# Optimization experiments

Measured on AMD Instinct MI355X. Metric: run time of the kernel, lower is better.

Reference implementation:

```python
import jax, jax.numpy as jnp
import numpy as np

T, B, N, F = 128, 8, 32, 128
H = 256  # hidden channels
DEG = 8


def setup_inputs() -> dict:
    key = jax.random.key(0)
    ks = jax.random.split(key, 8)
    data = jax.random.normal(ks[0], (T, B, N, F), jnp.float32)
    all_ohs = jax.random.normal(ks[1], (T, B, N, 8), jnp.float32)
    n0 = B * N * T
    n1 = B * N * (T // 2)
    edge_index0 = jax.random.randint(ks[2], (2, n0 * DEG), 0, n0)
    edge_index1 = jax.random.randint(ks[3], (2, n1 * DEG), 0, n1)
    def init(k, shape, fan):
        return jax.random.normal(k, shape, jnp.float32) / np.float32(np.sqrt(fan))
    W0 = init(ks[4], (2 * F, H), 2 * F); b0 = jnp.zeros((H,), jnp.float32)
    Wc0 = init(ks[5], (H, H, 5), H * 5); bc0 = jnp.zeros((H,), jnp.float32)
    W1 = init(ks[6], (2 * H, H), 2 * H); b1 = jnp.zeros((H,), jnp.float32)
    Wc1 = init(ks[7], (H, H, 5), H * 5); bc1 = jnp.zeros((H,), jnp.float32)
    return dict(data=data, all_ohs=all_ohs,
                edge_index0=edge_index0, edge_index1=edge_index1,
                W0=W0, b0=b0, Wc0=Wc0, bc0=bc0,
                W1=W1, b1=b1, Wc1=Wc1, bc1=bc1)


def edge_conv(x, edge_index, W, b):
    # PyG EdgeConv: out_i = max_{(j->i)} relu(Linear(cat[x_i, x_j - x_i]))
    src, dst = edge_index[0], edge_index[1]
    x_i = x[dst]           # [E, C] target features
    x_j = x[src]           # [E, C] source features
    msg = jax.nn.relu(jnp.concatenate([x_i, x_j - x_i], axis=-1) @ W + b)
    out = jax.ops.segment_max(msg, dst, num_segments=x.shape[0])
    return jnp.where(jnp.isneginf(out), 0.0, out)  # empty segments -> 0 (PyG fill)


def temp_conv(x, Wc, bc):
    # x: [BN, C, L]; Conv1d(k=5, pad=2) + relu + MaxPool1d(2)
    y = jax.lax.conv_general_dilated(x, Wc, (1,), [(2, 2)],
                                     dimension_numbers=('NCH', 'OIH', 'NCH'))
    y = jax.nn.relu(y + bc[None, :, None])
    L2 = y.shape[-1] // 2
    y = y[..., : L2 * 2].reshape(y.shape[0], y.shape[1], L2, 2)
    return jnp.max(y, axis=-1)


def reference(data, all_ohs, edge_index0, edge_index1,
              W0, b0, Wc0, bc0, W1, b1, Wc1, bc1):
    # 'fast' path, context=False: all_ohs unused beyond reshape
    length = data.shape[0]
    x = data.reshape(T, B * N, F).transpose(1, 0, 2).reshape(-1, F)  # [BN*T, F]
    layers = ((edge_index0, W0, b0, Wc0, bc0),
              (edge_index1, W1, b1, Wc1, bc1))
    for ei, W, b, Wc, bc in layers:
        x = edge_conv(x, ei, W, b)                       # [BN*length, C]
        x = x.reshape(-1, length, x.shape[-1])           # [BN, length, C]
        x = x.transpose(0, 2, 1)                         # [BN, C, length]
        x = temp_conv(x, Wc, bc)                         # [BN, C, length//2]
        length = x.shape[2]
        C = x.shape[1]
        x = x.transpose(0, 2, 1).reshape(-1, C)          # [BN*length, C]
    return x
```

## Files before the change

kernel.cpp:

```cpp
#include <hip/hip_runtime.h>
#include <hip/hip_bf16.h>
#include <math.h>

#define T0 128
#define BN 256
#define Ff 128
#define Hh 256
#define NODE0 32768
#define E0 262144
#define T1 64
#define NODE1 16384
#define E1 131072
#define CAP 48

typedef __attribute__((ext_vector_type(8))) short bhalf8;
typedef __attribute__((ext_vector_type(4))) float floatx4;
typedef __attribute__((ext_vector_type(16))) float floatx16;

__device__ __forceinline__ unsigned short f2bf(float x) {
  union { float f; unsigned u; } v; v.f = x;
  unsigned r = v.u + 0x7fff + ((v.u >> 16) & 1);
  return (unsigned short)(r >> 16);
}
__device__ __forceinline__ float bf2f(unsigned short b) {
  union { unsigned u; float f; } v; v.u = ((unsigned)b) << 16;
  return v.f;
}

__global__ void k_prepfill(const float* __restrict__ data, unsigned short* __restrict__ X0b,
                           const float* __restrict__ W0, unsigned short* __restrict__ Wbot0,
                           unsigned short* __restrict__ Wd0,
                           const float* __restrict__ W1, unsigned short* __restrict__ Wbot1,
                           unsigned short* __restrict__ Wd1,
                           const float* __restrict__ Wc0, unsigned short* __restrict__ Wtb0,
                           const float* __restrict__ Wc1, unsigned short* __restrict__ Wtb1,
                           const int* __restrict__ ei0, const int* __restrict__ ei1,
                           int* __restrict__ cnt0, int* __restrict__ cnt1,
                           int* __restrict__ slot0, int* __restrict__ slot1) {
  int b = blockIdx.x;
  int tid = threadIdx.x;
  if (b < 2048) {
    int idx = b * 256 + tid;
    int c8 = idx & 15;
    int r  = idx >> 4;
    int t  = r & (T0 - 1);
    int bn = r >> 7;
    const float* s = data + ((size_t)t * BN + bn) * Ff + c8 * 8;
    float4 a = *(const float4*)s;
    float4 bb = *(const float4*)(s + 4);
    unsigned short o[8];
    o[0] = f2bf(a.x); o[1] = f2bf(a.y); o[2] = f2bf(a.z); o[3] = f2bf(a.w);
    o[4] = f2bf(bb.x); o[5] = f2bf(bb.y); o[6] = f2bf(bb.z); o[7] = f2bf(bb.w);
    *(int4*)(X0b + ((size_t)(bn * T0 + t) * Ff + c8 * 8)) = *(int4*)o;
  } else if (b < 2176) {
    int idx = (b - 2048) * 256 + tid;
    int n = idx >> 7, k = idx & 127;
    float top = W0[(size_t)k * 256 + n];
    float bot = W0[(size_t)(128 + k) * 256 + n];
    Wbot0[idx] = f2bf(bot);
    Wd0[idx]   = f2bf(top - bot);
  } else if (b < 2432) {
    int idx = (b - 2176) * 256 + tid;
    int n = idx >> 8, k = idx & 255;
    float top = W1[(size_t)k * 256 + n];
    float bot = W1[(size_t)(256 + k) * 256 + n];
    Wbot1[idx] = f2bf(bot);
    Wd1[idx]   = f2bf(top - bot);
  } else if (b < 3712) {
    int idx = (b - 2432) * 256 + tid;
    int tap = idx >> 16, o = (idx >> 8) & 255, i = idx & 255;
    Wtb0[idx] = f2bf(Wc0[((size_t)o * 256 + i) * 5 + tap]);
  } else if (b < 4992) {
    int idx = (b - 3712) * 256 + tid;
    int tap = idx >> 16, o = (idx >> 8) & 255, i = idx & 255;
    Wtb1[idx] = f2bf(Wc1[((size_t)o * 256 + i) * 5 + tap]);
  } else {
    int e = (b - 4992) * 256 + tid;
    if (e < E0) {
      int d = ei0[E0 + e];
      int p = atomicAdd(&cnt0[d], 1);
      if (p < CAP) slot0[(size_t)d * CAP + p] = ei0[e];
    } else {
      int e2 = e - E0;
      int d = ei1[E1 + e2];
      int p = atomicAdd(&cnt1[d], 1);
      if (p < CAP) slot1[(size_t)d * CAP + p] = ei1[e2];
    }
  }
}

__global__ __launch_bounds__(256) void k_gemm2(const unsigned short* __restrict__ A,
                                               const unsigned short* __restrict__ Wbot,
                                               const unsigned short* __restrict__ Wd,
                                               unsigned short* __restrict__ Bm,
                                               unsigned short* __restrict__ P, int K,
                                               const float* __restrict__ bias) {
  __shared__ __align__(16) short A_lds[128 * 72];
  __shared__ __align__(16) short B0_lds[128 * 72];
  __shared__ __align__(16) short B1_lds[128 * 72];
  int tid = threadIdx.x;
  int row0 = blockIdx.x * 128;
  int col0 = blockIdx.y * 128;
  int lane = tid & 63, wv = tid >> 6;
  int m16 = lane & 15, quad = lane >> 4;
  int sr = tid >> 3, sseg = tid & 7;

  floatx4 accB[2][8], accP[2][8];
#pragma unroll
  for (int rt = 0; rt < 2; ++rt)
#pragma unroll
    for (int nt = 0; nt < 8; ++nt) {
      accB[rt][nt] = (floatx4){0.f, 0.f, 0.f, 0.f};
      accP[rt][nt] = (floatx4){0.f, 0.f, 0.f, 0.f};
    }

  for (int kb = 0; kb < K; kb += 64) {
    __syncthreads();
#pragma unroll
    for (int i = 0; i < 4; ++i) {
      int r = sr + i * 32;
      *(int4*)&A_lds[r * 72 + sseg * 8] =
          *(const int4*)(A + (size_t)(row0 + r) * K + kb + sseg * 8);
      *(int4*)&B0_lds[r * 72 + sseg * 8] =
          *(const int4*)(Wbot + (size_t)(col0 + r) * K + kb + sseg * 8);
      *(int4*)&B1_lds[r * 72 + sseg * 8] =
          *(const int4*)(Wd + (size_t)(col0 + r) * K + kb + sseg * 8);
    }
    __syncthreads();
#pragma unroll
    for (int ks = 0; ks < 2; ++ks) {
      bhalf8 a0 = *(const bhalf8*)&A_lds[(wv * 32 + m16) * 72 + ks * 32 + quad * 8];
      bhalf8 a1 = *(const bhalf8*)&A_lds[(wv * 32 + 16 + m16) * 72 + ks * 32 + quad * 8];
#pragma unroll
      for (int nt = 0; nt < 8; ++nt) {
        bhalf8 b0 = *(const bhalf8*)&B0_lds[(nt * 16 + m16) * 72 + ks * 32 + quad * 8];
        accB[0][nt] = __builtin_amdgcn_mfma_f32_16x16x32_bf16(a0, b0, accB[0][nt], 0, 0, 0);
        accB[1][nt] = __builtin_amdgcn_mfma_f32_16x16x32_bf16(a1, b0, accB[1][nt], 0, 0, 0);
        bhalf8 b1 = *(const bhalf8*)&B1_lds[(nt * 16 + m16) * 72 + ks * 32 + quad * 8];
        accP[0][nt] = __builtin_amdgcn_mfma_f32_16x16x32_bf16(a0, b1, accP[0][nt], 0, 0, 0);
        accP[1][nt] = __builtin_amdgcn_mfma_f32_16x16x32_bf16(a1, b1, accP[1][nt], 0, 0, 0);
      }
    }
  }

#pragma unroll
  for (int rt = 0; rt < 2; ++rt) {
    int g0 = row0 + wv * 32 + rt * 16 + quad * 4;
#pragma unroll
    for (int nt = 0; nt < 8; ++nt) {
      int c = col0 + nt * 16 + m16;
      float bv = bias[c];
#pragma unroll
      for (int r = 0; r < 4; ++r) {
        Bm[(size_t)(g0 + r) * 256 + c] = f2bf(accB[rt][nt][r]);
        P[(size_t)(g0 + r) * 256 + c]  = f2bf(accP[rt][nt][r] + bv);
      }
    }
  }
}

__global__ __launch_bounds__(256) void k_maxg2(const unsigned short* __restrict__ Bm,
                                               const int* __restrict__ cnt,
                                               const int* __restrict__ slot,
                                               const unsigned short* __restrict__ P,
                                               unsigned short* __restrict__ X1) {
  int node = blockIdx.x * 4 + (threadIdx.x >> 6);
  int lane = threadIdx.x & 63;
  int n = cnt[node];
  if (n > CAP) n = CAP;
  const int* sl = slot + (size_t)node * CAP;
  float4 m = make_float4(-INFINITY, -INFINITY, -INFINITY, -INFINITY);
  for (int i = 0; i < n; i += 8) {
    int s[8];
#pragma unroll
    for (int j = 0; j < 8; ++j) {
      int idx = i + j;
      s[j] = sl[(idx < n) ? idx : (n - 1)];
    }
    ushort4 v[8];
#pragma unroll
    for (int j = 0; j < 8; ++j)
      v[j] = *(const ushort4*)(Bm + (size_t)s[j] * 256 + lane * 4);
#pragma unroll
    for (int j = 0; j < 8; ++j) {
      m.x = fmaxf(m.x, bf2f(v[j].x));
      m.y = fmaxf(m.y, bf2f(v[j].y));
      m.z = fmaxf(m.z, bf2f(v[j].z));
      m.w = fmaxf(m.w, bf2f(v[j].w));
    }
  }
  ushort4 p = *(const ushort4*)(P + (size_t)node * 256 + lane * 4);
  ushort4 o;
  o.x = f2bf(fmaxf(bf2f(p.x) + m.x, 0.f));
  o.y = f2bf(fmaxf(bf2f(p.y) + m.y, 0.f));
  o.z = f2bf(fmaxf(bf2f(p.z) + m.z, 0.f));
  o.w = f2bf(fmaxf(bf2f(p.w) + m.w, 0.f));
  *(ushort4*)(X1 + (size_t)node * 256 + lane * 4) = o;
}

template <int TRows, int NT, bool OUT_F32>
__global__ __launch_bounds__(256) void k_conv32(const unsigned short* __restrict__ X,
                                                const unsigned short* __restrict__ Wtb,
                                                const float* __restrict__ bc,
                                                void* __restrict__ Yout) {
  const int CB = NT * 64;
  __shared__ __align__(16) short A_lds[2 * 68 * 40];
  __shared__ __align__(16) short B_lds[5 * CB * 40];
  int tid = threadIdx.x;
  int row0 = blockIdx.x * 128;
  int col0 = blockIdx.y * CB;
  int lane = tid & 63, wv = tid >> 6;
  int l31 = lane & 31, khalf = lane >> 5;
  int h = wv & 1, cpart = wv >> 1;

  floatx16 acc[2][NT];
#pragma unroll
  for (int rt = 0; rt < 2; ++rt)
#pragma unroll
    for (int ct = 0; ct < NT; ++ct)
#pragma unroll
      for (int r = 0; r < 16; ++r) acc[rt][ct][r] = 0.f;

  for (int kb = 0; kb < 256; kb += 32) {
    __syncthreads();
    for (int u = tid; u < 544; u += 256) {
      int s = (u >= 272) ? 1 : 0;
      int v = u - s * 272;
      int rr = v >> 2, seg = v & 3;
      int base = row0 + s * 64;
      int lo = base & ~(TRows - 1);
      int gr = base + rr - 2;
      int4 val = {0, 0, 0, 0};
      if (gr >= lo && gr < lo + TRows)
        val = *(const int4*)(X + (size_t)gr * 256 + kb + seg * 8);
      *(int4*)&A_lds[(s * 68 + rr) * 40 + seg * 8] = val;
    }
#pragma unroll
    for (int i = 0; i < 5 * NT; ++i) {
      int u = tid + i * 256;
      int r = u >> 2, seg = u & 3;
      int tap = r / CB, col = r % CB;
      *(int4*)&B_lds[r * 40 + seg * 8] =
          *(const int4*)(Wtb + (size_t)tap * 65536 + (size_t)(col0 + col) * 256 + kb + seg * 8);
    }
    __syncthreads();
#pragma unroll
    for (int tap = 0; tap < 5; ++tap) {
#pragma unroll
      for (int ks = 0; ks < 2; ++ks) {
        int ko = ks * 16 + khalf * 8;
        bhalf8 a[2];
#pragma unroll
        for (int rt = 0; rt < 2; ++rt)
          a[rt] = *(const bhalf8*)&A_lds[(h * 68 + rt * 32 + l31 + tap) * 40 + ko];
#pragma unroll
        for (int ct = 0; ct < NT; ++ct) {
          bhalf8 b = *(const bhalf8*)&B_lds[(tap * CB + cpart * NT * 32 + ct * 32 + l31) * 40 + ko];
#pragma unroll
          for (int rt = 0; rt < 2; ++rt)
            acc[rt][ct] = __builtin_amdgcn_mfma_f32_32x32x16_bf16(a[rt], b, acc[rt][ct], 0, 0, 0);
        }
      }
    }
  }

#pragma unroll
  for (int rt = 0; rt < 2; ++rt) {
#pragma unroll
    for (int ct = 0; ct < NT; ++ct) {
      int c = col0 + cpart * NT * 32 + ct * 32 + l31;
      float bv = bc[c];
#pragma unroll
      for (int r = 0; r < 16; r += 2) {
        int rowg = row0 + h * 64 + rt * 32 + 4 * khalf + 8 * (r >> 2) + (r & 3);
        float y0 = fmaxf(acc[rt][ct][r] + bv, 0.f);
        float y1 = fmaxf(acc[rt][ct][r + 1] + bv, 0.f);
        float p = fmaxf(y0, y1);
        int o = rowg >> 1;
        if (OUT_F32) ((float*)Yout)[(size_t)o * 256 + c] = p;
        else ((unsigned short*)Yout)[(size_t)o * 256 + c] = f2bf(p);
      }
    }
  }
}

extern "C" void kernel_launch(void* const* d_in, const int* in_sizes, int n_in,
                              void* d_out, int out_size, void* d_ws, size_t ws_size,
                              hipStream_t stream) {
  const float* data = (const float*)d_in[0];
  const int* ei0 = (const int*)d_in[2];
  const int* ei1 = (const int*)d_in[3];
  const float* W0  = (const float*)d_in[4];
  const float* b0  = (const float*)d_in[5];
  const float* Wc0 = (const float*)d_in[6];
  const float* bc0 = (const float*)d_in[7];
  const float* W1  = (const float*)d_in[8];
  const float* b1  = (const float*)d_in[9];
  const float* Wc1 = (const float*)d_in[10];
  const float* bc1 = (const float*)d_in[11];
  float* out = (float*)d_out;

  char* base = (char*)d_ws;
  size_t off = 0;
  auto alloc = [&](size_t bytes) { void* p = base + off; off += (bytes + 255) & ~(size_t)255; return p; };
  unsigned short* X0b   = (unsigned short*)alloc((size_t)NODE0 * Ff * 2);
  unsigned short* Bm    = (unsigned short*)alloc((size_t)NODE0 * Hh * 2);
  unsigned short* P     = (unsigned short*)alloc((size_t)NODE0 * Hh * 2);
  unsigned short* X1b   = (unsigned short*)alloc((size_t)NODE0 * Hh * 2);
  unsigned short* Y0b   = (unsigned short*)alloc((size_t)NODE1 * Hh * 2);
  unsigned short* Wbot0 = (unsigned short*)alloc(256 * 128 * 2);
  unsigned short* Wd0   = (unsigned short*)alloc(256 * 128 * 2);
  unsigned short* Wbot1 = (unsigned short*)alloc(256 * 256 * 2);
  unsigned short* Wd1   = (unsigned short*)alloc(256 * 256 * 2);
  unsigned short* Wtb0  = (unsigned short*)alloc(5 * 65536 * 2);
  unsigned short* Wtb1  = (unsigned short*)alloc(5 * 65536 * 2);
  int* cnt0  = (int*)alloc(NODE0 * 4);
  int* cnt1  = (int*)alloc(NODE1 * 4);
  int* slot0 = (int*)alloc((size_t)NODE0 * CAP * 4);
  int* slot1 = (int*)alloc((size_t)NODE1 * CAP * 4);

  hipMemsetAsync(cnt0, 0, (NODE0 + NODE1) * sizeof(int), stream);

  k_prepfill<<<6528, 256, 0, stream>>>(data, X0b, W0, Wbot0, Wd0, W1, Wbot1, Wd1,
                                       Wc0, Wtb0, Wc1, Wtb1,
                                       ei0, ei1, cnt0, cnt1, slot0, slot1);

  k_gemm2<<<dim3(NODE0 / 128, 2), 256, 0, stream>>>(X0b, Wbot0, Wd0, Bm, P, 128, b0);
  k_maxg2<<<NODE0 / 4, 256, 0, stream>>>(Bm, cnt0, slot0, P, X1b);
  k_conv32<128, 2, false><<<dim3(NODE0 / 128, 2), 256, 0, stream>>>(X1b, Wtb0, bc0, Y0b);

  k_gemm2<<<dim3(NODE1 / 128, 2), 256, 0, stream>>>(Y0b, Wbot1, Wd1, Bm, P, 256, b1);
  k_maxg2<<<NODE1 / 4, 256, 0, stream>>>(Bm, cnt1, slot1, P, X1b);
  k_conv32<64, 2, true><<<dim3(NODE1 / 128, 2), 256, 0, stream>>>(X1b, Wtb1, bc1, out);
}
```

Baseline: 219.7 us.

## Register-prefetch next K tile in GEMM and conv, vectorize gather-max and epilogue

Both the edge GEMM and the temporal-conv kernel now load the next K slice into registers while the current slice is being computed, so global-load latency overlaps the MFMA work. The GEMM swaps MFMA operand order so each lane holds four consecutive columns, which lets the epilogue write ushort4 vectors and read the bias as float4. The gather-max kernel loads 16-byte chunks with two half-waves taking alternating neighbours, then combines them with a cross-lane shuffle. The prefetch buffers raise register pressure, which may reduce occupancy, especially in the conv kernel with 5*NT prefetched int4 values.

```diff
diff --git a/kernel.cpp b/kernel.cpp
--- a/kernel.cpp
+++ b/kernel.cpp
@@ -25,6 +25,13 @@
 __device__ __forceinline__ float bf2f(unsigned short b) {
   union { unsigned u; float f; } v; v.u = ((unsigned)b) << 16;
   return v.f;
+}
+__device__ __forceinline__ void max2(float& mlo, float& mhi, int p) {
+  union { unsigned u; float f; } lo, hi;
+  lo.u = ((unsigned)p) << 16;
+  hi.u = ((unsigned)p) & 0xffff0000u;
+  mlo = fmaxf(mlo, lo.f);
+  mhi = fmaxf(mhi, hi.f);
 }
 
 __global__ void k_prepfill(const float* __restrict__ data, unsigned short* __restrict__ X0b,
@@ -105,6 +112,18 @@
   int m16 = lane & 15, quad = lane >> 4;
   int sr = tid >> 3, sseg = tid & 7;
 
+  const unsigned short* Abase  = A    + (size_t)(row0 + sr) * K + sseg * 8;
+  const unsigned short* B0base = Wbot + (size_t)(col0 + sr) * K + sseg * 8;
+  const unsigned short* B1base = Wd   + (size_t)(col0 + sr) * K + sseg * 8;
+
+  int4 ra[4], rb0[4], rb1[4];
+#pragma unroll
+  for (int i = 0; i < 4; ++i) {
+    ra[i]  = *(const int4*)(Abase  + (size_t)i * 32 * K);
+    rb0[i] = *(const int4*)(B0base + (size_t)i * 32 * K);
+    rb1[i] = *(const int4*)(B1base + (size_t)i * 32 * K);
+  }
+
   floatx4 accB[2][8], accP[2][8];
 #pragma unroll
   for (int rt = 0; rt < 2; ++rt)
@@ -119,12 +138,17 @@
 #pragma unroll
     for (int i = 0; i < 4; ++i) {
       int r = sr + i * 32;
-      *(int4*)&A_lds[r * 72 + sseg * 8] =
-          *(const int4*)(A + (size_t)(row0 + r) * K + kb + sseg * 8);
-      *(int4*)&B0_lds[r * 72 + sseg * 8] =
-          *(const int4*)(Wbot + (size_t)(col0 + r) * K + kb + sseg * 8);
-      *(int4*)&B1_lds[r * 72 + sseg * 8] =
-          *(const int4*)(Wd + (size_t)(col0 + r) * K + kb + sseg * 8);
+      *(int4*)&A_lds[r * 72 + sseg * 8]  = ra[i];
+      *(int4*)&B0_lds[r * 72 + sseg * 8] = rb0[i];
+      *(int4*)&B1_lds[r * 72 + sseg * 8] = rb1[i];
+    }
+    if (kb + 64 < K) {
+#pragma unroll
+      for (int i = 0; i < 4; ++i) {
+        ra[i]  = *(const int4*)(Abase  + (size_t)i * 32 * K + kb + 64);
+        rb0[i] = *(const int4*)(B0base + (size_t)i * 32 * K + kb + 64);
+        rb1[i] = *(const int4*)(B1base + (size_t)i * 32 * K + kb + 64);
+      }
     }
     __syncthreads();
 #pragma unroll
@@ -134,27 +158,29 @@
 #pragma unroll
       for (int nt = 0; nt < 8; ++nt) {
         bhalf8 b0 = *(const bhalf8*)&B0_lds[(nt * 16 + m16) * 72 + ks * 32 + quad * 8];
-        accB[0][nt] = __builtin_amdgcn_mfma_f32_16x16x32_bf16(a0, b0, accB[0][nt], 0, 0, 0);
-        accB[1][nt] = __builtin_amdgcn_mfma_f32_16x16x32_bf16(a1, b0, accB[1][nt], 0, 0, 0);
+        accB[0][nt] = __builtin_amdgcn_mfma_f32_16x16x32_bf16(b0, a0, accB[0][nt], 0, 0, 0);
+        accB[1][nt] = __builtin_amdgcn_mfma_f32_16x16x32_bf16(b0, a1, accB[1][nt], 0, 0, 0);
         bhalf8 b1 = *(const bhalf8*)&B1_lds[(nt * 16 + m16) * 72 + ks * 32 + quad * 8];
-        accP[0][nt] = __builtin_amdgcn_mfma_f32_16x16x32_bf16(a0, b1, accP[0][nt], 0, 0, 0);
-        accP[1][nt] = __builtin_amdgcn_mfma_f32_16x16x32_bf16(a1, b1, accP[1][nt], 0, 0, 0);
+        accP[0][nt] = __builtin_amdgcn_mfma_f32_16x16x32_bf16(b1, a0, accP[0][nt], 0, 0, 0);
+        accP[1][nt] = __builtin_amdgcn_mfma_f32_16x16x32_bf16(b1, a1, accP[1][nt], 0, 0, 0);
       }
     }
   }
 
 #pragma unroll
   for (int rt = 0; rt < 2; ++rt) {
-    int g0 = row0 + wv * 32 + rt * 16 + quad * 4;
+    int row = row0 + wv * 32 + rt * 16 + m16;
 #pragma unroll
     for (int nt = 0; nt < 8; ++nt) {
-      int c = col0 + nt * 16 + m16;
-      float bv = bias[c];
-#pragma unroll
-      for (int r = 0; r < 4; ++r) {
-        Bm[(size_t)(g0 + r) * 256 + c] = f2bf(accB[rt][nt][r]);
-        P[(size_t)(g0 + r) * 256 + c]  = f2bf(accP[rt][nt][r] + bv);
-      }
+      int c = col0 + nt * 16 + quad * 4;
+      float4 bv = *(const float4*)&bias[c];
+      ushort4 ob, op;
+      ob.x = f2bf(accB[rt][nt][0]); ob.y = f2bf(accB[rt][nt][1]);
+      ob.z = f2bf(accB[rt][nt][2]); ob.w = f2bf(accB[rt][nt][3]);
+      op.x = f2bf(accP[rt][nt][0] + bv.x); op.y = f2bf(accP[rt][nt][1] + bv.y);
+      op.z = f2bf(accP[rt][nt][2] + bv.z); op.w = f2bf(accP[rt][nt][3] + bv.w);
+      *(ushort4*)(Bm + (size_t)row * 256 + c) = ob;
+      *(ushort4*)(P  + (size_t)row * 256 + c) = op;
     }
   }
 }
@@ -166,36 +192,52 @@
                                                unsigned short* __restrict__ X1) {
   int node = blockIdx.x * 4 + (threadIdx.x >> 6);
   int lane = threadIdx.x & 63;
+  int half = lane >> 5, c8 = lane & 31;
   int n = cnt[node];
   if (n > CAP) n = CAP;
   const int* sl = slot + (size_t)node * CAP;
-  float4 m = make_float4(-INFINITY, -INFINITY, -INFINITY, -INFINITY);
+  float m[8];
+#pragma unroll
+  for (int e = 0; e < 8; ++e) m[e] = -INFINITY;
   for (int i = 0; i < n; i += 8) {
-    int s[8];
-#pragma unroll
-    for (int j = 0; j < 8; ++j) {
-      int idx = i + j;
+    int s[4];
+#pragma unroll
+    for (int j = 0; j < 4; ++j) {
+      int idx = i + 2 * j + half;
       s[j] = sl[(idx < n) ? idx : (n - 1)];
     }
-    ushort4 v[8];
-#pragma unroll
-    for (int j = 0; j < 8; ++j)
-      v[j] = *(const ushort4*)(Bm + (size_t)s[j] * 256 + lane * 4);
-#pragma unroll
-    for (int j = 0; j < 8; ++j) {
-      m.x = fmaxf(m.x, bf2f(v[j].x));
-      m.y = fmaxf(m.y, bf2f(v[j].y));
-      m.z = fmaxf(m.z, bf2f(v[j].z));
-      m.w = fmaxf(m.w, bf2f(v[j].w));
-    }
-  }
-  ushort4 p = *(const ushort4*)(P + (size_t)node * 256 + lane * 4);
-  ushort4 o;
-  o.x = f2bf(fmaxf(bf2f(p.x) + m.x, 0.f));
-  o.y = f2bf(fmaxf(bf2f(p.y) + m.y, 0.f));
-  o.z = f2bf(fmaxf(bf2f(p.z) + m.z, 0.f));
-  o.w = f2bf(fmaxf(bf2f(p.w) + m.w, 0.f));
-  *(ushort4*)(X1 + (size_t)node * 256 + lane * 4) = o;
+    int4 v[4];
+#pragma unroll
+    for (int j = 0; j < 4; ++j)
+      v[j] = *(const int4*)(Bm + (size_t)s[j] * 256 + c8 * 8);
+#pragma unroll
+    for (int j = 0; j < 4; ++j) {
+      max2(m[0], m[1], v[j].x);
+      max2(m[2], m[3], v[j].y);
+      max2(m[4], m[5], v[j].z);
+      max2(m[6], m[7], v[j].w);
+    }
+  }
+#pragma unroll
+  for (int e = 0; e < 8; ++e) m[e] = fmaxf(m[e], __shfl_xor(m[e], 32));
+  if (half == 0) {
+    int4 p = *(const int4*)(P + (size_t)node * 256 + c8 * 8);
+    int4 o;
+    unsigned short r0, r1;
+    r0 = f2bf(fmaxf(bf2f((unsigned short)(p.x & 0xffff)) + m[0], 0.f));
+    r1 = f2bf(fmaxf(bf2f((unsigned short)((unsigned)p.x >> 16)) + m[1], 0.f));
+    o.x = (int)r0 | ((int)r1 << 16);
+    r0 = f2bf(fmaxf(bf2f((unsigned short)(p.y & 0xffff)) + m[2], 0.f));
+    r1 = f2bf(fmaxf(bf2f((unsigned short)((unsigned)p.y >> 16)) + m[3], 0.f));
+    o.y = (int)r0 | ((int)r1 << 16);
+    r0 = f2bf(fmaxf(bf2f((unsigned short)(p.z & 0xffff)) + m[4], 0.f));
+    r1 = f2bf(fmaxf(bf2f((unsigned short)((unsigned)p.z >> 16)) + m[5], 0.f));
+    o.z = (int)r0 | ((int)r1 << 16);
+    r0 = f2bf(fmaxf(bf2f((unsigned short)(p.w & 0xffff)) + m[6], 0.f));
+    r1 = f2bf(fmaxf(bf2f((unsigned short)((unsigned)p.w >> 16)) + m[7], 0.f));
+    o.w = (int)r0 | ((int)r1 << 16);
+    *(int4*)(X1 + (size_t)node * 256 + c8 * 8) = o;
+  }
 }
 
 template <int TRows, int NT, bool OUT_F32>
@@ -213,6 +255,38 @@
   int l31 = lane & 31, khalf = lane >> 5;
   int h = wv & 1, cpart = wv >> 1;
 
+  bool av[3]; int alds[3]; const unsigned short* aptr[3]; bool ain[3];
+#pragma unroll
+  for (int j = 0; j < 3; ++j) {
+    int u = tid + j * 256;
+    av[j] = (u < 544);
+    int s = (u >= 272) ? 1 : 0;
+    int v = u - s * 272;
+    int rr = v >> 2, seg = v & 3;
+    int base = row0 + s * 64;
+    int lo = base & ~(TRows - 1);
+    int gr = base + rr - 2;
+    alds[j] = (s * 68 + rr) * 40 + seg * 8;
+    ain[j] = av[j] && (gr >= lo) && (gr < lo + TRows);
+    aptr[j] = X + (size_t)gr * 256 + seg * 8;
+  }
+  int blds[5 * NT]; const unsigned short* bptr[5 * NT];
+#pragma unroll
+  for (int i = 0; i < 5 * NT; ++i) {
+    int u = tid + i * 256;
+    int r = u >> 2, seg = u & 3;
+    int tap = r / CB, col = r % CB;
+    blds[i] = r * 40 + seg * 8;
+    bptr[i] = Wtb + (size_t)tap * 65536 + (size_t)(col0 + col) * 256 + seg * 8;
+  }
+
+  int4 pa[3], pb[5 * NT];
+#pragma unroll
+  for (int j = 0; j < 3; ++j)
+    pa[j] = ain[j] ? *(const int4*)(aptr[j]) : (int4){0, 0, 0, 0};
+#pragma unroll
+  for (int i = 0; i < 5 * NT; ++i) pb[i] = *(const int4*)(bptr[i]);
+
   floatx16 acc[2][NT];
 #pragma unroll
   for (int rt = 0; rt < 2; ++rt)
@@ -223,25 +297,17 @@
 
   for (int kb = 0; kb < 256; kb += 32) {
     __syncthreads();
-    for (int u = tid; u < 544; u += 256) {
-      int s = (u >= 272) ? 1 : 0;
-      int v = u - s * 272;
-      int rr = v >> 2, seg = v & 3;
-      int base = row0 + s * 64;
-      int lo = base & ~(TRows - 1);
-      int gr = base + rr - 2;
-      int4 val = {0, 0, 0, 0};
-      if (gr >= lo && gr < lo + TRows)
-        val = *(const int4*)(X + (size_t)gr * 256 + kb + seg * 8);
-      *(int4*)&A_lds[(s * 68 + rr) * 40 + seg * 8] = val;
-    }
-#pragma unroll
-    for (int i = 0; i < 5 * NT; ++i) {
-      int u = tid + i * 256;
-      int r = u >> 2, seg = u & 3;
-      int tap = r / CB, col = r % CB;
-      *(int4*)&B_lds[r * 40 + seg * 8] =
-          *(const int4*)(Wtb + (size_t)tap * 65536 + (size_t)(col0 + col) * 256 + kb + seg * 8);
+#pragma unroll
+    for (int j = 0; j < 3; ++j)
+      if (av[j]) *(int4*)&A_lds[alds[j]] = pa[j];
+#pragma unroll
+    for (int i = 0; i < 5 * NT; ++i) *(int4*)&B_lds[blds[i]] = pb[i];
+    if (kb + 32 < 256) {
+#pragma unroll
+      for (int j = 0; j < 3; ++j)
+        pa[j] = ain[j] ? *(const int4*)(aptr[j] + kb + 32) : (int4){0, 0, 0, 0};
+#pragma unroll
+      for (int i = 0; i < 5 * NT; ++i) pb[i] = *(const int4*)(bptr[i] + kb + 32);
     }
     __syncthreads();
 #pragma unroll
```

Result: slower. 334.7 us (+52.3%).
